# Kernel tuning notes

Hardware: AMD Instinct MI355X
Metric: run time of the kernel (lower is better)

The kernel has to match this reference:

```python
import jax, jax.numpy as jnp
import numpy as np

N_FREQS = 10
EPS = 1e-5

def embed(p):
    # NeRF positional embedding: [p, sin(p*2^0), cos(p*2^0), ..., sin(p*2^9), cos(p*2^9)]
    freqs = 2.0 ** jnp.arange(N_FREQS, dtype=p.dtype)  # [10]
    ang = p[:, :, None] * freqs[None, None, :]          # [N,3,10]
    sc = jnp.stack([jnp.sin(ang), jnp.cos(ang)], axis=-1)  # [N,3,10,2]
    return jnp.concatenate([p, sc.reshape(p.shape[0], -1)], axis=-1)  # [N, 63]

def edge_conv(x, edge_index, w1, b1, w2, b2):
    src, dst = edge_index[0], edge_index[1]
    xi = x[dst]                                # target features [E, F]
    h = jnp.concatenate([xi, x[src] - xi], -1)  # [E, 2F]
    h = jax.nn.relu(h @ w1 + b1) @ w2 + b2      # [E, out]
    n = x.shape[0]
    s = jax.ops.segment_sum(h, dst, num_segments=n)
    cnt = jax.ops.segment_sum(jnp.ones((h.shape[0],), h.dtype), dst, num_segments=n)
    return s / jnp.clip(cnt, 1.0)[:, None]      # mean aggregation

def batch_norm(x, gamma, beta):
    mu = jnp.mean(x, axis=0)
    var = jnp.mean((x - mu) ** 2, axis=0)
    return (x - mu) * jax.lax.rsqrt(var + EPS) * gamma + beta

def distribute_features(features, face_indices, num_vertices):
    n, f = features.shape
    feat = features.reshape(n * 3, f // 3)
    idx = face_indices.reshape(-1)
    vsum = jax.ops.segment_sum(feat, idx, num_segments=num_vertices)
    cnt = jax.ops.segment_sum(jnp.ones((idx.shape[0],), feat.dtype), idx, num_segments=num_vertices)
    vmean = vsum / jnp.clip(cnt, 1.0)[:, None]
    return vmean[idx].reshape(n, f)

def _mlp_params(key, in_dim, out_dim):
    k1, k2, k3, k4 = jax.random.split(key, 4)
    h = 2 * out_dim
    return (jax.random.normal(k1, (2 * in_dim, h), jnp.float32) * (1.0 / np.sqrt(2 * in_dim)),
            jax.random.normal(k2, (h,), jnp.float32) * 0.01,
            jax.random.normal(k3, (h, out_dim), jnp.float32) * (1.0 / np.sqrt(h)),
            jax.random.normal(k4, (out_dim,), jnp.float32) * 0.01)

def setup_inputs() -> dict:
    key = jax.random.key(0)
    ks = jax.random.split(key, 10)
    N, E, V = 100000, 300000, 50000
    inp = {
        'x': jax.random.normal(ks[0], (N, 16), jnp.float32),
        'edge_index': jax.random.randint(ks[1], (2, E), 0, N, jnp.int32),
        'faces': jax.random.randint(ks[2], (N, 3), 0, V, jnp.int32),
        'num_vertices': V,
    }
    dims = [(196, 96), (96, 192), (192, 384), (384, 384), (384, 576)]
    for i, (di, do) in enumerate(dims, start=1):
        w1, b1, w2, b2 = _mlp_params(ks[2 + i], di, do)
        inp[f'gc{i}_w1'], inp[f'gc{i}_b1'], inp[f'gc{i}_w2'], inp[f'gc{i}_b2'] = w1, b1, w2, b2
    for i, d in enumerate([96, 192, 384, 384], start=1):
        inp[f'gamma{i}'] = jnp.ones((d,), jnp.float32)
        inp[f'beta{i}'] = jnp.zeros((d,), jnp.float32)
    return inp

def reference(x, edge_index, faces, num_vertices,
              gc1_w1, gc1_b1, gc1_w2, gc1_b2,
              gc2_w1, gc2_b1, gc2_w2, gc2_b2,
              gc3_w1, gc3_b1, gc3_w2, gc3_b2,
              gc4_w1, gc4_b1, gc4_w2, gc4_b2,
              gc5_w1, gc5_b1, gc5_w2, gc5_b2,
              gamma1, beta1, gamma2, beta2, gamma3, beta3, gamma4, beta4):
    h = jnp.concatenate([embed(x[:, :3]), embed(x[:, 3:6]), embed(x[:, 6:9]), x[:, 9:]], -1)  # [N,196]
    h = jax.nn.relu(batch_norm(edge_conv(h, edge_index, gc1_w1, gc1_b1, gc1_w2, gc1_b2), gamma1, beta1))
    h = distribute_features(h, faces, num_vertices)
    h = jax.nn.relu(batch_norm(edge_conv(h, edge_index, gc2_w1, gc2_b1, gc2_w2, gc2_b2), gamma2, beta2))
    h = distribute_features(h, faces, num_vertices)
    h = jax.nn.relu(batch_norm(edge_conv(h, edge_index, gc3_w1, gc3_b1, gc3_w2, gc3_b2), gamma3, beta3))
    h = distribute_features(h, faces, num_vertices)
    h = jax.nn.relu(batch_norm(edge_conv(h, edge_index, gc4_w1, gc4_b1, gc4_w2, gc4_b2), gamma4, beta4))
    h = distribute_features(h, faces, num_vertices)
    h = edge_conv(h, edge_index, gc5_w1, gc5_b1, gc5_w2, gc5_b2)
    h = distribute_features(h, faces, num_vertices)
    return h
```

## Files before the change

kernel.cpp:

```cpp
#include <hip/hip_runtime.h>
#include <hip/hip_bf16.h>
#include <stdint.h>


typedef __hip_bfloat16 bf16;
typedef __attribute__((ext_vector_type(8))) short bf16x8;
typedef __attribute__((ext_vector_type(4))) float f32x4;
#define CHUNK 384

static inline int cdiv(int a, int b) { return (a + b - 1) / b; }

__device__ __forceinline__ float bf2f(bf16 v) { return __bfloat162float(v); }
__device__ __forceinline__ bf16 f2bf(float v) { return __float2bfloat16(v); }
__device__ __forceinline__ unsigned short f2bs(float v) {
  bf16 h = __float2bfloat16(v);
  return *reinterpret_cast<unsigned short*>(&h);
}

__device__ __forceinline__ void gload16(const bf16* g, bf16* lds_base) {
  __builtin_amdgcn_global_load_lds((const __attribute__((address_space(1))) void*)g,
                                   (__attribute__((address_space(3))) void*)lds_base,
                                   16, 0, 0);
}

__device__ __forceinline__ void swz_decode(int T, int nn, int& mb, int& nb) {
  int i = blockIdx.x;
  int q = T >> 3, r = T & 7;
  int xcd = i & 7, rank = i >> 3;
  int wg = (xcd < r ? xcd * (q + 1) : r * (q + 1) + (xcd - r) * q) + rank;
  nb = wg % nn;
  mb = wg / nn;
}

__global__ __launch_bounds__(256) void k_embed(const float* __restrict__ x,
                                               bf16* __restrict__ h, int N) {
  int idx = blockIdx.x * 256 + threadIdx.x;
  if (idx >= N * 224) return;
  int n = idx / 224;
  int c = idx - n * 224;
  float v = 0.f;
  if (c >= 196) {
    v = 0.f;
  } else if (c >= 189) {
    v = x[n * 16 + 9 + (c - 189)];
  } else {
    int g = c / 63;
    int cc = c - g * 63;
    const float* p = x + n * 16 + g * 3;
    if (cc < 3) {
      v = p[cc];
    } else {
      int t = cc - 3;
      int comp = t / 20;
      int rem = t - comp * 20;
      float ang = p[comp] * (float)(1 << (rem >> 1));
      v = (rem & 1) ? cosf(ang) : sinf(ang);
    }
  }
  h[idx] = f2bf(v);
}

__global__ __launch_bounds__(256) void k_count(const int* __restrict__ idxs,
                                               int* __restrict__ deg, int M) {
  int i = blockIdx.x * 256 + threadIdx.x;
  if (i < M) atomicAdd(&deg[idxs[i]], 1);
}

__global__ __launch_bounds__(256) void k_recip(const int* __restrict__ deg,
                                               float* __restrict__ r, int n) {
  int i = blockIdx.x * 256 + threadIdx.x;
  if (i < n) {
    int d = deg[i];
    r[i] = d > 0 ? 1.f / (float)d : 0.f;
  }
}

__global__ __launch_bounds__(1024) void k_scan(const int* __restrict__ deg,
                                               int* __restrict__ off,
                                               int* __restrict__ cursor, int n) {
  __shared__ int part[1024];
  int t = threadIdx.x;
  int per = (n + 1023) / 1024;
  int b = t * per;
  int e = b + per;
  if (b > n) b = n;
  if (e > n) e = n;
  int s = 0;
  for (int i = b; i < e; ++i) s += deg[i];
  part[t] = s;
  __syncthreads();
  if (t == 0) {
    int r = 0;
    for (int i = 0; i < 1024; ++i) {
      int x = part[i];
      part[i] = r;
      r += x;
    }
    off[n] = r;
  }
  __syncthreads();
  int r = part[t];
  for (int i = b; i < e; ++i) {
    off[i] = r;
    cursor[i] = r;
    r += deg[i];
  }
}

__global__ __launch_bounds__(256) void k_fill_edges(const int* __restrict__ ei, int E,
                                                    int* __restrict__ cursor,
                                                    int* __restrict__ esrc) {
  int e = blockIdx.x * 256 + threadIdx.x;
  if (e >= E) return;
  int dst = ei[E + e];
  int pos = atomicAdd(&cursor[dst], 1);
  esrc[pos] = ei[e];
}

__global__ __launch_bounds__(256) void k_fill_faces(const int* __restrict__ faces, int M,
                                                    int* __restrict__ cursor,
                                                    int* __restrict__ vidx) {
  int i = blockIdx.x * 256 + threadIdx.x;
  if (i >= M) return;
  int v = faces[i];
  int pos = atomicAdd(&cursor[v], 1);
  vidx[pos] = i;
}

__global__ __launch_bounds__(256) void k_prep_w1(const float* __restrict__ w1,
                                                 bf16* __restrict__ WdT,
                                                 bf16* __restrict__ WbT,
                                                 int F, int H, int F_pad, int H_pad) {
  int idx = blockIdx.x * 256 + threadIdx.x;
  if (idx >= H_pad * F_pad) return;
  int n = idx / F_pad;
  int k = idx - n * F_pad;
  float vd = 0.f, vb = 0.f;
  if (n < H && k < F) {
    float top = w1[(size_t)k * H + n];
    float bot = w1[(size_t)(F + k) * H + n];
    vd = top - bot;
    vb = bot;
  }
  WdT[idx] = f2bf(vd);
  WbT[idx] = f2bf(vb);
}

__global__ __launch_bounds__(256) void k_prep_w2(const float* __restrict__ w2,
                                                 bf16* __restrict__ W2T, int H, int O,
                                                 int O_pad) {
  int idx = blockIdx.x * 256 + threadIdx.x;
  if (idx >= O_pad * H) return;
  int n = idx / H;
  int k = idx - n * H;
  float v = (n < O) ? w2[(size_t)k * O + n] : 0.f;
  W2T[idx] = f2bf(v);
}

__global__ __launch_bounds__(256) void gemm1_mfma(
    const bf16* __restrict__ A, int lda,
    const bf16* __restrict__ WdT, const bf16* __restrict__ WbT,
    const float* __restrict__ b1, int c0,
    bf16* __restrict__ outC, bf16* __restrict__ outB,
    int N, int K_pad, int Hc, int nn) {
  __shared__ bf16 sA[128 * 32];
  __shared__ bf16 sBd[128 * 32];
  __shared__ bf16 sBb[128 * 32];
  int mb, nb;
  swz_decode(gridDim.x, nn, mb, nb);
  const int tid = threadIdx.x;
  const int lane = tid & 63, wv = tid >> 6;
  const int wm = wv & 1, wn = wv >> 1;
  const int lr = lane & 15, quad = lane >> 4;
  const int m_blk = mb * 128, n_blk = nb * 128;
  const int rs = lane >> 2;
  const int cg = (lane & 3) ^ ((lane >> 3) & 3);
  const int gsw = (quad ^ ((lr >> 1) & 3)) << 3;
  f32x4 accC[4][4], accB[4][4];
#pragma unroll
  for (int i = 0; i < 4; ++i)
#pragma unroll
    for (int j = 0; j < 4; ++j) {
      accC[i][j] = (f32x4){0.f, 0.f, 0.f, 0.f};
      accB[i][j] = (f32x4){0.f, 0.f, 0.f, 0.f};
    }
  const int kTiles = K_pad >> 5;
  for (int kt = 0; kt < kTiles; ++kt) {
    const int k0 = (kt << 5) + cg * 8;
#pragma unroll
    for (int i = 0; i < 2; ++i) {
      const int rb = wv * 32 + i * 16;
      const int ro = rb + rs;
      gload16(A + (size_t)(m_blk + ro) * lda + k0, &sA[rb * 32]);
      gload16(WdT + (size_t)(n_blk + ro) * K_pad + k0, &sBd[rb * 32]);
      gload16(WbT + (size_t)(n_blk + ro) * K_pad + k0, &sBb[rb * 32]);
    }
    __syncthreads();
    bf16x8 af[4];
#pragma unroll
    for (int im = 0; im < 4; ++im)
      af[im] = *(const bf16x8*)&sA[(wm * 64 + im * 16 + lr) * 32 + gsw];
#pragma unroll
    for (int jn = 0; jn < 4; ++jn) {
      int go = (wn * 64 + jn * 16 + lr) * 32 + gsw;
      bf16x8 bd = *(const bf16x8*)&sBd[go];
      bf16x8 bb = *(const bf16x8*)&sBb[go];
#pragma unroll
      for (int im = 0; im < 4; ++im) {
        accC[im][jn] = __builtin_amdgcn_mfma_f32_16x16x32_bf16(af[im], bd, accC[im][jn], 0, 0, 0);
        accB[im][jn] = __builtin_amdgcn_mfma_f32_16x16x32_bf16(af[im], bb, accB[im][jn], 0, 0, 0);
      }
    }
    __syncthreads();
  }
#pragma unroll
  for (int jn = 0; jn < 4; ++jn) {
    int c = n_blk + wn * 64 + jn * 16 + lr;
    if (c >= Hc) continue;
    float bv = b1[c0 + c];
#pragma unroll
    for (int im = 0; im < 4; ++im) {
      int mb2 = m_blk + wm * 64 + im * 16 + quad * 4;
#pragma unroll
      for (int rg = 0; rg < 4; ++rg) {
        int r = mb2 + rg;
        if (r >= N) continue;
        size_t o = (size_t)r * Hc + c;
        outC[o] = f2bf(accC[im][jn][rg] + bv);
        outB[o] = f2bf(accB[im][jn][rg]);
      }
    }
  }
}

__global__ __launch_bounds__(256) void gemm2_mfma(
    const bf16* __restrict__ S, int ldS,
    const bf16* __restrict__ W2T, int ldw,
    const float* __restrict__ b2, const float* __restrict__ rdeg,
    float* __restrict__ Eo, float* __restrict__ stats, int do_stats,
    int N, int K, int O, int nn) {
  __shared__ bf16 sA[128 * 32];
  __shared__ bf16 sB[128 * 32];
  int mb, nb;
  swz_decode(gridDim.x, nn, mb, nb);
  const int tid = threadIdx.x;
  const int lane = tid & 63, wv = tid >> 6;
  const int wm = wv & 1, wn = wv >> 1;
  const int lr = lane & 15, quad = lane >> 4;
  const int m_blk = mb * 128, n_blk = nb * 128;
  const int rs = lane >> 2;
  const int cg = (lane & 3) ^ ((lane >> 3) & 3);
  const int gsw = (quad ^ ((lr >> 1) & 3)) << 3;
  f32x4 acc[4][4];
#pragma unroll
  for (int i = 0; i < 4; ++i)
#pragma unroll
    for (int j = 0; j < 4; ++j) acc[i][j] = (f32x4){0.f, 0.f, 0.f, 0.f};
  const int kTiles = K >> 5;
  for (int kt = 0; kt < kTiles; ++kt) {
    const int k0 = (kt << 5) + cg * 8;
#pragma unroll
    for (int i = 0; i < 2; ++i) {
      const int rb = wv * 32 + i * 16;
      const int ro = rb + rs;
      gload16(S + (size_t)(m_blk + ro) * ldS + k0, &sA[rb * 32]);
      gload16(W2T + (size_t)(n_blk + ro) * ldw + k0, &sB[rb * 32]);
    }
    __syncthreads();
    bf16x8 af[4];
#pragma unroll
    for (int im = 0; im < 4; ++im)
      af[im] = *(const bf16x8*)&sA[(wm * 64 + im * 16 + lr) * 32 + gsw];
#pragma unroll
    for (int jn = 0; jn < 4; ++jn) {
      bf16x8 bb = *(const bf16x8*)&sB[(wn * 64 + jn * 16 + lr) * 32 + gsw];
#pragma unroll
      for (int im = 0; im < 4; ++im)
        acc[im][jn] = __builtin_amdgcn_mfma_f32_16x16x32_bf16(af[im], bb, acc[im][jn], 0, 0, 0);
    }
    __syncthreads();
  }
#pragma unroll
  for (int jn = 0; jn < 4; ++jn) {
    int c = n_blk + wn * 64 + jn * 16 + lr;
    if (c >= O) continue;
    float b2v = b2[c];
    float ssum = 0.f, qsum = 0.f;
#pragma unroll
    for (int im = 0; im < 4; ++im) {
      int mb2 = m_blk + wm * 64 + im * 16 + quad * 4;
#pragma unroll
      for (int rg = 0; rg < 4; ++rg) {
        int r = mb2 + rg;
        if (r >= N) continue;
        float rd = rdeg[r];
        float v = acc[im][jn][rg] * rd;
        if (rd != 0.f) v += b2v;
        Eo[(size_t)r * O + c] = v;
        ssum += v;
        qsum += v * v;
      }
    }
    if (do_stats) {
      ssum += __shfl_xor(ssum, 16);
      ssum += __shfl_xor(ssum, 32);
      qsum += __shfl_xor(qsum, 16);
      qsum += __shfl_xor(qsum, 32);
      if (quad == 0) {
        unsafeAtomicAdd(&stats[c], ssum);
        unsafeAtomicAdd(&stats[O + c], qsum);
      }
    }
  }
}

__global__ __launch_bounds__(256) void k_edge_gather(
    const int* __restrict__ eoff, const int* __restrict__ esrc,
    const bf16* __restrict__ C, const bf16* __restrict__ B,
    bf16* __restrict__ S, int ldS, int c0, int N, int Hc) {
  int gw = (blockIdx.x * 256 + threadIdx.x) >> 6;
  int lane = threadIdx.x & 63;
  if (gw >= N) return;
  int beg = eoff[gw], end = eoff[gw + 1];
  const uint32_t* Crow = reinterpret_cast<const uint32_t*>(C + (size_t)gw * Hc);
  float cc0[3], cc1[3], acc0[3], acc1[3];
#pragma unroll
  for (int w = 0; w < 3; ++w) {
    acc0[w] = 0.f;
    acc1[w] = 0.f;
    cc0[w] = 0.f;
    cc1[w] = 0.f;
    int j2 = lane + w * 64;
    if (j2 * 2 < Hc) {
      uint32_t uc = Crow[j2];
      cc0[w] = __uint_as_float(uc << 16);
      cc1[w] = __uint_as_float(uc & 0xffff0000u);
    }
  }
  for (int e = beg; e < end; ++e) {
    int src = esrc[e];
    const uint32_t* Brow = reinterpret_cast<const uint32_t*>(B + (size_t)src * Hc);
#pragma unroll
    for (int w = 0; w < 3; ++w) {
      int j2 = lane + w * 64;
      if (j2 * 2 < Hc) {
        uint32_t ub = Brow[j2];
        acc0[w] += fmaxf(cc0[w] + __uint_as_float(ub << 16), 0.f);
        acc1[w] += fmaxf(cc1[w] + __uint_as_float(ub & 0xffff0000u), 0.f);
      }
    }
  }
  uint32_t* Srow = reinterpret_cast<uint32_t*>(S + (size_t)gw * ldS + c0);
#pragma unroll
  for (int w = 0; w < 3; ++w) {
    int j2 = lane + w * 64;
    if (j2 * 2 < Hc)
      Srow[j2] = ((uint32_t)f2bs(acc1[w]) << 16) | (uint32_t)f2bs(acc0[w]);
  }
}

__global__ __launch_bounds__(256) void k_bn_finalize(const float* __restrict__ stats,
                                                     const float* __restrict__ gamma,
                                                     const float* __restrict__ beta,
                                                     float* __restrict__ scale,
                                                     float* __restrict__ shift, int N, int O) {
  int c = blockIdx.x * 256 + threadIdx.x;
  if (c >= O) return;
  float mu = stats[c] / (float)N;
  float var = stats[O + c] / (float)N - mu * mu;
  float sc = gamma[c] * rsqrtf(var + 1e-5f);
  scale[c] = sc;
  shift[c] = beta[c] - mu * sc;
}

__global__ __launch_bounds__(256) void k_vgather(
    const int* __restrict__ voff, const int* __restrict__ vidx,
    const float* __restrict__ Ef, const float* __restrict__ scale,
    const float* __restrict__ shift, int use_bn,
    float* __restrict__ Vf, int V, int O, int O3) {
  int idx = blockIdx.x * 256 + threadIdx.x;
  if (idx >= V * O3) return;
  int v = idx / O3;
  int c = idx - v * O3;
  int beg = voff[v], end = voff[v + 1];
  float acc = 0.f;
  for (int e = beg; e < end; ++e) {
    int i = vidx[e];
    int n = i / 3;
    int g = i - n * 3;
    int col = g * O3 + c;
    float x = Ef[(size_t)n * O + col];
    if (use_bn) x = fmaxf(fmaf(x, scale[col], shift[col]), 0.f);
    acc += x;
  }
  Vf[idx] = acc;
}

__global__ __launch_bounds__(256) void k_gather_bf16(const float* __restrict__ Vf,
                                                     const int* __restrict__ faces,
                                                     const float* __restrict__ rv,
                                                     bf16* __restrict__ out,
                                                     int N, int O, int O3) {
  int idx = blockIdx.x * 256 + threadIdx.x;
  if (idx >= N * O) return;
  int n = idx / O;
  int c = idx - n * O;
  int g = c / O3;
  int vert = faces[n * 3 + g];
  out[idx] = f2bf(Vf[(size_t)vert * O3 + (c - g * O3)] * rv[vert]);
}

__global__ __launch_bounds__(256) void k_gather_f32(const float* __restrict__ Vf,
                                                    const int* __restrict__ faces,
                                                    const float* __restrict__ rv,
                                                    float* __restrict__ out,
                                                    int N, int O, int O3) {
  int idx = blockIdx.x * 256 + threadIdx.x;
  if (idx >= N * O) return;
  int n = idx / O;
  int c = idx - n * O;
  int g = c / O3;
  int vert = faces[n * 3 + g];
  out[idx] = Vf[(size_t)vert * O3 + (c - g * O3)] * rv[vert];
}

extern "C" void kernel_launch(void* const* d_in, const int* in_sizes, int n_in,
                              void* d_out, int out_size, void* d_ws, size_t ws_size,
                              hipStream_t stream) {
  (void)n_in; (void)out_size; (void)ws_size;
  const float* x = (const float*)d_in[0];
  const int* ei = (const int*)d_in[1];
  const int* faces = (const int*)d_in[2];
  const int N = in_sizes[0] / 16;
  const int E = in_sizes[1] / 2;
  const int V = 50000;
  const int N_pad = cdiv(N, 128) * 128;

  char* p = (char*)d_ws;
  auto carve = [&](size_t bytes) -> char* {
    char* r = p;
    p += (bytes + 255) & ~(size_t)255;
    return r;
  };
  bf16* buf_h = (bf16*)carve((size_t)N_pad * 384 * sizeof(bf16));
  float* buf_e = (float*)carve((size_t)N * 384 * sizeof(float));
  bf16* buf_C = (bf16*)carve((size_t)N * CHUNK * sizeof(bf16));
  bf16* buf_B = (bf16*)carve((size_t)N * CHUNK * sizeof(bf16));
  bf16* buf_S = (bf16*)carve((size_t)N_pad * 1152 * sizeof(bf16));
  float* buf_V = (float*)carve((size_t)V * 192 * sizeof(float));
  bf16* buf_WdT = (bf16*)carve((size_t)1050000 * sizeof(bf16));
  bf16* buf_WbT = (bf16*)carve((size_t)1050000 * sizeof(bf16));
  bf16* buf_W2T = (bf16*)carve((size_t)1500000 * sizeof(bf16));
  int* ideg = (int*)carve((size_t)N * 4);
  int* ivdeg = (int*)carve((size_t)V * 4);
  float* rdegN = (float*)carve((size_t)N * 4);
  float* rdegV = (float*)carve((size_t)V * 4);
  float* stats = (float*)carve(2 * 576 * 4);
  float* scale = (float*)carve(576 * 4);
  float* shift = (float*)carve(576 * 4);
  int* e_off = (int*)carve((size_t)(N + 1) * 4);
  int* e_cur = (int*)carve((size_t)N * 4);
  int* e_src = (int*)carve((size_t)E * 4);
  int* v_off = (int*)carve((size_t)(V + 1) * 4);
  int* v_cur = (int*)carve((size_t)V * 4);
  int* v_idx = (int*)carve((size_t)3 * N * 4);

  hipMemsetAsync(ideg, 0, (size_t)N * 4, stream);
  hipMemsetAsync(ivdeg, 0, (size_t)V * 4, stream);
  k_count<<<cdiv(E, 256), 256, 0, stream>>>(ei + E, ideg, E);
  k_count<<<cdiv(3 * N, 256), 256, 0, stream>>>(faces, ivdeg, 3 * N);
  k_recip<<<cdiv(N, 256), 256, 0, stream>>>(ideg, rdegN, N);
  k_recip<<<cdiv(V, 256), 256, 0, stream>>>(ivdeg, rdegV, V);

  k_scan<<<1, 1024, 0, stream>>>(ideg, e_off, e_cur, N);
  k_scan<<<1, 1024, 0, stream>>>(ivdeg, v_off, v_cur, V);
  k_fill_edges<<<cdiv(E, 256), 256, 0, stream>>>(ei, E, e_cur, e_src);
  k_fill_faces<<<cdiv(3 * N, 256), 256, 0, stream>>>(faces, 3 * N, v_cur, v_idx);

  k_embed<<<cdiv(N * 224, 256), 256, 0, stream>>>(x, buf_h, N);

  const int LF[5] = {196, 96, 192, 384, 384};
  const int LH[5] = {192, 384, 768, 768, 1152};
  const int LO[5] = {96, 192, 384, 384, 576};

  size_t off1 = 0, off2 = 0;
  const int nm = cdiv(N, 128);

  for (int l = 0; l < 5; ++l) {
    const int F = LF[l], H = LH[l], O = LO[l], O3 = O / 3;
    const int F_pad = ((F + 31) / 32) * 32;
    int Hc_last = H % CHUNK;
    if (Hc_last == 0) Hc_last = CHUNK;
    const int H_pad = H - Hc_last + cdiv(Hc_last, 128) * 128;
    const int O_pad = cdiv(O, 128) * 128;
    const float* w1 = (const float*)d_in[4 + l * 4];
    const float* b1 = (const float*)d_in[5 + l * 4];
    const float* w2 = (const float*)d_in[6 + l * 4];
    const float* b2 = (const float*)d_in[7 + l * 4];
    float* Ebuf = (l == 4) ? (float*)d_out : buf_e;
    bf16* WdT = buf_WdT + off1;
    bf16* WbT = buf_WbT + off1;
    bf16* W2T = buf_W2T + off2;
    off1 += (size_t)H_pad * F_pad;
    off2 += (size_t)O_pad * H;

    k_prep_w1<<<cdiv(H_pad * F_pad, 256), 256, 0, stream>>>(w1, WdT, WbT, F, H, F_pad, H_pad);
    k_prep_w2<<<cdiv(O_pad * H, 256), 256, 0, stream>>>(w2, W2T, H, O, O_pad);

    for (int c0 = 0; c0 < H; c0 += CHUNK) {
      int Hc = (H - c0 < CHUNK) ? (H - c0) : CHUNK;
      int nn1 = cdiv(Hc, 128);
      gemm1_mfma<<<nm * nn1, 256, 0, stream>>>(buf_h, F_pad,
                                               WdT + (size_t)c0 * F_pad, WbT + (size_t)c0 * F_pad,
                                               b1, c0, buf_C, buf_B, N, F_pad, Hc, nn1);
      k_edge_gather<<<cdiv(N * 64, 256), 256, 0, stream>>>(e_off, e_src, buf_C, buf_B,
                                                           buf_S, H, c0, N, Hc);
    }

    if (l < 4) hipMemsetAsync(stats, 0, (size_t)2 * O * 4, stream);
    int nn2 = cdiv(O, 128);
    gemm2_mfma<<<nm * nn2, 256, 0, stream>>>(buf_S, H, W2T, H, b2, rdegN, Ebuf,
                                             stats, (l < 4) ? 1 : 0, N, H, O, nn2);

    if (l < 4)
      k_bn_finalize<<<cdiv(O, 256), 256, 0, stream>>>(
          stats, (const float*)d_in[24 + l * 2], (const float*)d_in[25 + l * 2],
          scale, shift, N, O);

    k_vgather<<<cdiv(V * O3, 256), 256, 0, stream>>>(v_off, v_idx, Ebuf, scale, shift,
                                                     (l < 4) ? 1 : 0, buf_V, V, O, O3);
    if (l < 4)
      k_gather_bf16<<<cdiv(N * O, 256), 256, 0, stream>>>(buf_V, faces, rdegV, buf_h, N, O, O3);
    else
      k_gather_f32<<<cdiv(N * O, 256), 256, 0, stream>>>(buf_V, faces, rdegV, (float*)d_out, N, O, O3);
  }
}
```

Before: 5.034 ms.

## Double-buffer LDS tiles in both MFMA GEMMs to overlap loads with compute

Both GEMM kernels now keep two LDS buffers and issue the global-to-LDS loads for the next K tile before computing the current one. A single vmcnt wait plus barrier per iteration replaces the two __syncthreads. The intent is to hide global load latency behind MFMA work. LDS use doubles, which may lower occupancy. gemm2 also preloads the rdeg values into registers before the epilogue instead of reloading them for each column.

```diff
diff --git a/kernel.cpp b/kernel.cpp
--- a/kernel.cpp
+++ b/kernel.cpp
@@ -22,6 +22,8 @@
                                    (__attribute__((address_space(3))) void*)lds_base,
                                    16, 0, 0);
 }
+
+#define WAIT_VM0 asm volatile("s_waitcnt vmcnt(0)" ::: "memory")
 
 __device__ __forceinline__ void swz_decode(int T, int nn, int& mb, int& nb) {
   int i = blockIdx.x;
@@ -163,9 +165,9 @@
     const float* __restrict__ b1, int c0,
     bf16* __restrict__ outC, bf16* __restrict__ outB,
     int N, int K_pad, int Hc, int nn) {
-  __shared__ bf16 sA[128 * 32];
-  __shared__ bf16 sBd[128 * 32];
-  __shared__ bf16 sBb[128 * 32];
+  __shared__ bf16 sA[2][128 * 32];
+  __shared__ bf16 sBd[2][128 * 32];
+  __shared__ bf16 sBb[2][128 * 32];
   int mb, nb;
   swz_decode(gridDim.x, nn, mb, nb);
   const int tid = threadIdx.x;
@@ -184,35 +186,50 @@
       accC[i][j] = (f32x4){0.f, 0.f, 0.f, 0.f};
       accB[i][j] = (f32x4){0.f, 0.f, 0.f, 0.f};
     }
-  const int kTiles = K_pad >> 5;
-  for (int kt = 0; kt < kTiles; ++kt) {
+
+  auto stage = [&](int kt, int buf) {
     const int k0 = (kt << 5) + cg * 8;
 #pragma unroll
     for (int i = 0; i < 2; ++i) {
       const int rb = wv * 32 + i * 16;
       const int ro = rb + rs;
-      gload16(A + (size_t)(m_blk + ro) * lda + k0, &sA[rb * 32]);
-      gload16(WdT + (size_t)(n_blk + ro) * K_pad + k0, &sBd[rb * 32]);
-      gload16(WbT + (size_t)(n_blk + ro) * K_pad + k0, &sBb[rb * 32]);
-    }
-    __syncthreads();
+      gload16(A + (size_t)(m_blk + ro) * lda + k0, &sA[buf][rb * 32]);
+      gload16(WdT + (size_t)(n_blk + ro) * K_pad + k0, &sBd[buf][rb * 32]);
+      gload16(WbT + (size_t)(n_blk + ro) * K_pad + k0, &sBb[buf][rb * 32]);
+    }
+  };
+  auto compute = [&](int buf) {
     bf16x8 af[4];
 #pragma unroll
     for (int im = 0; im < 4; ++im)
-      af[im] = *(const bf16x8*)&sA[(wm * 64 + im * 16 + lr) * 32 + gsw];
+      af[im] = *(const bf16x8*)&sA[buf][(wm * 64 + im * 16 + lr) * 32 + gsw];
 #pragma unroll
     for (int jn = 0; jn < 4; ++jn) {
       int go = (wn * 64 + jn * 16 + lr) * 32 + gsw;
-      bf16x8 bd = *(const bf16x8*)&sBd[go];
-      bf16x8 bb = *(const bf16x8*)&sBb[go];
+      bf16x8 bd = *(const bf16x8*)&sBd[buf][go];
+      bf16x8 bb = *(const bf16x8*)&sBb[buf][go];
 #pragma unroll
       for (int im = 0; im < 4; ++im) {
         accC[im][jn] = __builtin_amdgcn_mfma_f32_16x16x32_bf16(af[im], bd, accC[im][jn], 0, 0, 0);
         accB[im][jn] = __builtin_amdgcn_mfma_f32_16x16x32_bf16(af[im], bb, accB[im][jn], 0, 0, 0);
       }
     }
-    __syncthreads();
-  }
+  };
+
+  const int kTiles = K_pad >> 5;
+  stage(0, 0);
+  WAIT_VM0;
+  __builtin_amdgcn_s_barrier();
+  int cur = 0;
+  for (int kt = 0; kt < kTiles - 1; ++kt) {
+    stage(kt + 1, cur ^ 1);
+    compute(cur);
+    WAIT_VM0;
+    __builtin_amdgcn_s_barrier();
+    cur ^= 1;
+  }
+  compute(cur);
+
 #pragma unroll
   for (int jn = 0; jn < 4; ++jn) {
     int c = n_blk + wn * 64 + jn * 16 + lr;
@@ -239,8 +256,8 @@
     const float* __restrict__ b2, const float* __restrict__ rdeg,
     float* __restrict__ Eo, float* __restrict__ stats, int do_stats,
     int N, int K, int O, int nn) {
-  __shared__ bf16 sA[128 * 32];
-  __shared__ bf16 sB[128 * 32];
+  __shared__ bf16 sA[2][128 * 32];
+  __shared__ bf16 sB[2][128 * 32];
   int mb, nb;
   swz_decode(gridDim.x, nn, mb, nb);
   const int tid = threadIdx.x;
@@ -256,29 +273,54 @@
   for (int i = 0; i < 4; ++i)
 #pragma unroll
     for (int j = 0; j < 4; ++j) acc[i][j] = (f32x4){0.f, 0.f, 0.f, 0.f};
-  const int kTiles = K >> 5;
-  for (int kt = 0; kt < kTiles; ++kt) {
+
+  auto stage = [&](int kt, int buf) {
     const int k0 = (kt << 5) + cg * 8;
 #pragma unroll
     for (int i = 0; i < 2; ++i) {
       const int rb = wv * 32 + i * 16;
       const int ro = rb + rs;
-      gload16(S + (size_t)(m_blk + ro) * ldS + k0, &sA[rb * 32]);
-      gload16(W2T + (size_t)(n_blk + ro) * ldw + k0, &sB[rb * 32]);
-    }
-    __syncthreads();
+      gload16(S + (size_t)(m_blk + ro) * ldS + k0, &sA[buf][rb * 32]);
+      gload16(W2T + (size_t)(n_blk + ro) * ldw + k0, &sB[buf][rb * 32]);
+    }
+  };
+  auto compute = [&](int buf) {
     bf16x8 af[4];
 #pragma unroll
     for (int im = 0; im < 4; ++im)
-      af[im] = *(const bf16x8*)&sA[(wm * 64 + im * 16 + lr) * 32 + gsw];
+      af[im] = *(const bf16x8*)&sA[buf][(wm * 64 + im * 16 + lr) * 32 + gsw];
 #pragma unroll
     for (int jn = 0; jn < 4; ++jn) {
-      bf16x8 bb = *(const bf16x8*)&sB[(wn * 64 + jn * 16 + lr) * 32 + gsw];
+      bf16x8 bb = *(const bf16x8*)&sB[buf][(wn * 64 + jn * 16 + lr) * 32 + gsw];
 #pragma unroll
       for (int im = 0; im < 4; ++im)
         acc[im][jn] = __builtin_amdgcn_mfma_f32_16x16x32_bf16(af[im], bb, acc[im][jn], 0, 0, 0);
     }
-    __syncthreads();
+  };
+
+  const int kTiles = K >> 5;
+  stage(0, 0);
+  WAIT_VM0;
+  __builtin_amdgcn_s_barrier();
+  int cur = 0;
+  for (int kt = 0; kt < kTiles - 1; ++kt) {
+    stage(kt + 1, cur ^ 1);
+    compute(cur);
+    WAIT_VM0;
+    __builtin_amdgcn_s_barrier();
+    cur ^= 1;
+  }
+  compute(cur);
+
+  float rdv[4][4];
+#pragma unroll
+  for (int im = 0; im < 4; ++im) {
+    int mb2 = m_blk + wm * 64 + im * 16 + quad * 4;
+#pragma unroll
+    for (int rg = 0; rg < 4; ++rg) {
+      int r = mb2 + rg;
+      rdv[im][rg] = (r < N) ? rdeg[r] : 0.f;
+    }
   }
 #pragma unroll
   for (int jn = 0; jn < 4; ++jn) {
@@ -293,7 +335,7 @@
       for (int rg = 0; rg < 4; ++rg) {
         int r = mb2 + rg;
         if (r >= N) continue;
-        float rd = rdeg[r];
+        float rd = rdv[im][rg];
         float v = acc[im][jn][rg] * rd;
         if (rd != 0.f) v += b2v;
         Eo[(size_t)r * O + c] = v;
```

Measured after the change: 4.542 ms. 9.8% less time.
